# Performance work log

Measured on AMD Instinct MI355X. Metric: run time of the kernel, lower is better.

## Reference

```python
import jax, jax.numpy as jnp
import numpy as np

NEG_CAUSAL = -1e10  # matches torch buffer triu(ones*-1e10, diag=1)
NEG_PAD = -10000.0
NUM_HEADS = 16


def setup_inputs() -> dict:
    key = jax.random.key(0)
    ks = jax.random.split(key, 6)
    B, S, D = 2, 2048, 1024
    scale = 0.02
    return {
        "hidden_states": jax.random.normal(ks[0], (B, S, D), jnp.float32),
        "attention_mask": jnp.ones((B, S), jnp.float32),
        "Wq": jax.random.normal(ks[1], (D, D), jnp.float32) * scale,
        "bq": jnp.zeros((D,), jnp.float32),
        "Wk": jax.random.normal(ks[2], (D, D), jnp.float32) * scale,
        "bk": jnp.zeros((D,), jnp.float32),
        "Wv": jax.random.normal(ks[3], (D, D), jnp.float32) * scale,
        "bv": jnp.zeros((D,), jnp.float32),
        "Wo": jax.random.normal(ks[4], (D, D), jnp.float32) * scale,
        "bo": jnp.zeros((D,), jnp.float32),
    }


def reference(hidden_states, attention_mask, Wq, bq, Wk, bk, Wv, bv, Wo, bo):
    B, S, D = hidden_states.shape
    H = NUM_HEADS
    hd = D // H

    def heads(x):  # [B,S,D] -> [B,H,S,hd]
        return x.reshape(B, S, H, hd).transpose(0, 2, 1, 3)

    q = heads(hidden_states @ Wq + bq)
    k = heads(hidden_states @ Wk + bk)
    v = heads(hidden_states @ Wv + bv)

    scores = jnp.einsum("bhqd,bhkd->bhqk", q, k) / jnp.sqrt(jnp.float32(hd))
    causal = jnp.triu(jnp.full((S, S), NEG_CAUSAL, jnp.float32), k=1)
    scores = scores + causal
    # additive padding mask: (1 - m) * -10000, broadcast over heads and query pos
    scores = scores + (1.0 - attention_mask)[:, None, None, :] * NEG_PAD

    probs = jax.nn.softmax(scores, axis=-1)
    # dropout p=0.1 is inactive in eval mode (training=False)
    ctx = jnp.einsum("bhqk,bhkd->bhqd", probs, v)
    ctx = ctx.transpose(0, 2, 1, 3).reshape(B, S, D)
    return ctx @ Wo + bo
```

## Files before the change

### kernel.cpp

```cpp
#include <hip/hip_runtime.h>

typedef __attribute__((ext_vector_type(8))) short short8_t;
typedef __attribute__((ext_vector_type(4))) float float4_t;
typedef unsigned short u16;
typedef unsigned int u32;
typedef unsigned long long u64;

__device__ inline u16 f2bf(float x) {
  union { float f; u32 u; } v; v.f = x;
  u32 r = v.u + 0x7FFFu + ((v.u >> 16) & 1u);
  return (u16)(r >> 16);
}
#if __has_builtin(__builtin_amdgcn_cvt_pk_bf16_f32)
typedef __attribute__((ext_vector_type(2))) __bf16 bf162_t;
__device__ inline u32 pk2(float a, float b) {
  union { bf162_t v; u32 u; } cv;
  cv.v = __builtin_amdgcn_cvt_pk_bf16_f32(a, b);
  return cv.u;
}
#else
__device__ inline u32 pk2(float a, float b) {
  return (u32)f2bf(a) | ((u32)f2bf(b) << 16);
}
#endif

__global__ __launch_bounds__(256) void prologue(const float* __restrict__ X,
                                                const float* __restrict__ Wq, const float* __restrict__ Wk,
                                                const float* __restrict__ Wv, const float* __restrict__ Wo,
                                                u16* __restrict__ Xb, u16* __restrict__ WqkvT,
                                                u16* __restrict__ WoT, const float* __restrict__ maskp,
                                                u32* __restrict__ flags) {
  __shared__ float tls[32][33];
  int bid = blockIdx.x;
  if (bid < 4096) {
    int i = bid * 256 + threadIdx.x;
    float4_t x = ((const float4_t*)X)[i];
    union { u32 u[2]; u64 ll; } o;
    o.u[0] = pk2(x[0], x[1]);
    o.u[1] = pk2(x[2], x[3]);
    ((u64*)Xb)[i] = o.ll;
  } else if (bid < 8192) {
    int t = bid - 4096;
    int mat = t >> 10, tile = t & 1023;
    const float* W = (mat == 0) ? Wq : (mat == 1) ? Wk : (mat == 2) ? Wv : Wo;
    u16* WT = (mat < 3) ? WqkvT + ((size_t)mat << 20) : WoT;
    int tx = threadIdx.x & 31, ty = threadIdx.x >> 5;
    int c0 = (tile & 31) * 32, r0 = (tile >> 5) * 32;
    #pragma unroll
    for (int i = 0; i < 4; ++i)
      tls[ty + i * 8][tx] = W[(r0 + ty + i * 8) * 1024 + c0 + tx];
    __syncthreads();
    #pragma unroll
    for (int i = 0; i < 4; ++i)
      WT[(size_t)(c0 + ty + i * 8) * 1024 + r0 + tx] = f2bf(tls[tx][ty + i * 8]);
  } else {
    int b = bid - 8192;
    const float* mb = maskp + (b << 11) + threadIdx.x * 8;
    bool ok = true;
    #pragma unroll
    for (int i = 0; i < 8; ++i) ok &= (mb[i] == 1.0f);
    u64 bal = __ballot(ok);
    int w = threadIdx.x >> 6;
    if ((threadIdx.x & 63) == 0) tls[0][w] = (bal == ~0ull) ? 1.0f : 0.0f;
    __syncthreads();
    if (threadIdx.x == 0)
      flags[b] = (tls[0][0] != 0.0f && tls[0][1] != 0.0f &&
                  tls[0][2] != 0.0f && tls[0][3] != 0.0f) ? 1u : 0u;
  }
}

__global__ __launch_bounds__(256) void gemm128(const u16* __restrict__ A, const u16* __restrict__ BT,
                                               const float* __restrict__ bias0, const float* __restrict__ bias1,
                                               const float* __restrict__ bias2,
                                               void* __restrict__ o0, void* __restrict__ o1, void* __restrict__ o2,
                                               int mode) {
  __shared__ __align__(16) u16 Als[128 * 64];
  __shared__ __align__(16) u16 Bls[128 * 64];
  int g = blockIdx.x, m0t, n0t;
  if (mode == 4) {
    int mh = g / 384, r = g - mh * 384;
    n0t = r >> 4;
    m0t = mh * 16 + (r & 15);
  } else {
    m0t = g & 31;
    n0t = g >> 5;
  }
  const int m0 = m0t * 128, n0 = n0t * 128;
  const int lane = threadIdx.x & 63, wave = threadIdx.x >> 6;
  const int quad = lane >> 4, c = lane & 15;
  const int wm = wave >> 1, wn = wave & 1;

  const int srow = lane >> 3, schunk = lane & 7;
  int soff[4], dst[4];
  #pragma unroll
  for (int q = 0; q < 4; ++q) {
    int r = wave * 32 + q * 8 + srow;
    soff[q] = r * 1024 + (schunk << 3);
    dst[q]  = r * 64 + ((schunk ^ (r & 7)) << 3);
  }
  const u16* gA = A + (size_t)m0 * 1024;
  const u16* gB = BT + (size_t)n0 * 1024;

  int ar[2][4], br[2][4];
  #pragma unroll
  for (int ko = 0; ko < 2; ++ko) {
    #pragma unroll
    for (int i = 0; i < 4; ++i) {
      int rowa = wm * 64 + i * 16 + c;
      ar[ko][i] = rowa * 64 + (((ko * 4 + quad) ^ (rowa & 7)) << 3);
      int rowb = wn * 64 + i * 16 + c;
      br[ko][i] = rowb * 64 + (((ko * 4 + quad) ^ (rowb & 7)) << 3);
    }
  }

  short8_t ra[4], rb[4];
  #pragma unroll
  for (int q = 0; q < 4; ++q) ra[q] = *(const short8_t*)(gA + soff[q]);
  #pragma unroll
  for (int q = 0; q < 4; ++q) rb[q] = *(const short8_t*)(gB + soff[q]);

  float4_t acc[4][4] = {};
  for (int k0 = 0; k0 < 1024; k0 += 64) {
    #pragma unroll
    for (int q = 0; q < 4; ++q) *(short8_t*)&Als[dst[q]] = ra[q];
    #pragma unroll
    for (int q = 0; q < 4; ++q) *(short8_t*)&Bls[dst[q]] = rb[q];
    __syncthreads();
    if (k0 < 960) {
      #pragma unroll
      for (int q = 0; q < 4; ++q) ra[q] = *(const short8_t*)(gA + soff[q] + k0 + 64);
      #pragma unroll
      for (int q = 0; q < 4; ++q) rb[q] = *(const short8_t*)(gB + soff[q] + k0 + 64);
    }
    #pragma unroll
    for (int ko = 0; ko < 2; ++ko) {
      short8_t af[4], bfr[4];
      #pragma unroll
      for (int i = 0; i < 4; ++i) af[i] = *(const short8_t*)&Als[ar[ko][i]];
      #pragma unroll
      for (int j = 0; j < 4; ++j) bfr[j] = *(const short8_t*)&Bls[br[ko][j]];
      #pragma unroll
      for (int i = 0; i < 4; ++i)
        #pragma unroll
        for (int j = 0; j < 4; ++j)
          acc[i][j] = __builtin_amdgcn_mfma_f32_16x16x32_bf16(af[i], bfr[j], acc[i][j], 0, 0, 0);
    }
    __syncthreads();
  }

  const int mrow = m0 + wm * 64, ncol = n0 + wn * 64;
  if (mode == 3) {
    float* o = (float*)o0;
    #pragma unroll
    for (int i = 0; i < 4; ++i) {
      #pragma unroll
      for (int j = 0; j < 4; ++j) {
        int colb = ncol + j * 16 + c;
        float bv = bias0[colb];
        int rowb = mrow + i * 16 + quad * 4;
        #pragma unroll
        for (int r = 0; r < 4; ++r)
          o[(size_t)(rowb + r) * 1024 + colb] = acc[i][j][r] + bv;
      }
    }
  } else {
    #pragma unroll
    for (int j = 0; j < 4; ++j) {
      int colb = ncol + j * 16 + c;
      int which = colb >> 10;
      int n1 = colb & 1023, h = n1 >> 6, d = n1 & 63;
      const float* bp = (which == 0) ? bias0 : (which == 1 ? bias1 : bias2);
      float bv = bp[n1];
      #pragma unroll
      for (int i = 0; i < 4; ++i) {
        int rowb = mrow + i * 16 + quad * 4;
        int b = rowb >> 11, s = rowb & 2047;
        if (which == 2) {
          u16* o = (u16*)o2 + (((size_t)(b * 16 + h) * 64 + d) * 2048 + s);
          union { u32 u[2]; u64 ll; } ov;
          ov.u[0] = pk2(acc[i][j][0] + bv, acc[i][j][1] + bv);
          ov.u[1] = pk2(acc[i][j][2] + bv, acc[i][j][3] + bv);
          *(u64*)o = ov.ll;
        } else {
          float sc = (which == 0) ? 0.18033688011112042f : 1.0f;
          u16* o = (u16*)((which == 0) ? o0 : o1);
          #pragma unroll
          for (int r = 0; r < 4; ++r)
            o[(((size_t)(b * 16 + h) * 2048 + (s + r)) << 6) + d] = f2bf((acc[i][j][r] + bv) * sc);
        }
      }
    }
  }
}

__device__ inline short8_t p_to_b_swap(const float* p) {
  u32 a0 = pk2(p[0], p[1]), a1 = pk2(p[2], p[3]);
  u32 b0 = pk2(p[4], p[5]), b1 = pk2(p[6], p[7]);
  asm("v_permlane32_swap_b32 %0, %1" : "+v"(a0), "+v"(b0));
  asm("v_permlane32_swap_b32 %0, %1" : "+v"(a1), "+v"(b1));
  asm("v_permlane16_swap_b32 %0, %1" : "+v"(a0), "+v"(b0));
  asm("v_permlane16_swap_b32 %0, %1" : "+v"(a1), "+v"(b1));
  union { u32 u[4]; short8_t v; } pf;
  pf.u[0] = a0; pf.u[1] = a1; pf.u[2] = b0; pf.u[3] = b1;
  return pf.v;
}

__global__ __launch_bounds__(256, 4) void attn_kernel(const u16* __restrict__ Q, const u16* __restrict__ K,
                                                      const u16* __restrict__ VT, const float* __restrict__ mask,
                                                      const u32* __restrict__ flags, u16* __restrict__ ctx) {
  __shared__ __align__(16) u16 Kls[2 * 64 * 64];
  __shared__ __align__(16) u16 Vls[2 * 64 * 64];
  const float C1 = 10000.0f * 1.4426950408889634f;
  int w = threadIdx.x >> 6, lane = threadIdx.x & 63;
  int quad = lane >> 4, c = lane & 15;
  int g = blockIdx.x;
  int bh = (g & 7) * 4 + ((g >> 3) & 3);
  int u = g >> 5;
  int qt = (u < 16) ? (31 - u) : (u - 16);
  int b = bh >> 4, h = bh & 15;
  bool ones = flags && (flags[b] != 0);
  const u16* Kp = K + ((size_t)bh << 17);
  const u16* Vp = VT + ((size_t)bh << 17);
  const float* mp = mask + (b << 11);
  int q0 = qt * 64 + w * 16;

  const u16* Qp = Q + (((size_t)bh * 2048 + q0 + c) << 6) + quad * 8;
  short8_t qf0 = *(const short8_t*)(Qp);
  short8_t qf1 = *(const short8_t*)(Qp + 32);

  const int srow = lane >> 3, schunk = lane & 7;
  const u16* gK[2]; const u16* gV[2]; int dK[2], dV[2];
  #pragma unroll
  for (int i = 0; i < 2; ++i) {
    int R = w * 16 + i * 8 + srow;
    gK[i] = Kp + R * 64 + (schunk << 3);
    dK[i] = R * 64 + ((schunk ^ (R & 7)) << 3);
    gV[i] = Vp + (size_t)R * 2048 + (schunk << 3);
    dV[i] = R * 64 + ((schunk ^ (R & 7)) << 3);
  }

  int koff[4][2];
  #pragma unroll
  for (int kg = 0; kg < 4; ++kg) {
    int r = kg * 16 + c;
    #pragma unroll
    for (int ko = 0; ko < 2; ++ko)
      koff[kg][ko] = r * 64 + (((ko * 4 + quad) ^ (r & 7)) << 3);
  }
  int voff[4][2];
  #pragma unroll
  for (int dblk = 0; dblk < 4; ++dblk) {
    int d = dblk * 16 + c;
    #pragma unroll
    for (int kc = 0; kc < 2; ++kc)
      voff[dblk][kc] = d * 64 + (((kc * 4 + quad) ^ (d & 7)) << 3);
  }

  int ke[8];
  #pragma unroll
  for (int e = 0; e < 8; ++e) ke[e] = ((e >> 2) << 4) + quad * 4 + (e & 3);
  int thr = w * 16 + c;

  float4_t O[4] = {};
  float l = 0.0f;

  short8_t kreg[2], vreg[2];
  #pragma unroll
  for (int i = 0; i < 2; ++i) { kreg[i] = *(const short8_t*)(gK[i]); vreg[i] = *(const short8_t*)(gV[i]); }

  for (int t = 0; t <= qt; ++t) {
    int kb = t << 6;
    int bufo = (t & 1) << 12;
    #pragma unroll
    for (int i = 0; i < 2; ++i) *(short8_t*)&Kls[bufo + dK[i]] = kreg[i];
    #pragma unroll
    for (int i = 0; i < 2; ++i) *(short8_t*)&Vls[bufo + dV[i]] = vreg[i];
    __syncthreads();
    if (t < qt) {
      int kb2 = (t + 1) << 6;
      #pragma unroll
      for (int i = 0; i < 2; ++i) {
        kreg[i] = *(const short8_t*)(gK[i] + (size_t)kb2 * 64);
        vreg[i] = *(const short8_t*)(gV[i] + kb2);
      }
    }
    float4_t s[4];
    #pragma unroll
    for (int kg = 0; kg < 4; ++kg) {
      short8_t k0 = *(const short8_t*)&Kls[bufo + koff[kg][0]];
      short8_t k1 = *(const short8_t*)&Kls[bufo + koff[kg][1]];
      float4_t a = {};
      a = __builtin_amdgcn_mfma_f32_16x16x32_bf16(k0, qf0, a, 0, 0, 0);
      a = __builtin_amdgcn_mfma_f32_16x16x32_bf16(k1, qf1, a, 0, 0, 0);
      s[kg] = a;
    }
    float4_t mpl[4];
    if (!ones) {
      #pragma unroll
      for (int kg = 0; kg < 4; ++kg)
        mpl[kg] = (*(const float4_t*)(mp + kb + kg * 16 + quad * 4) - 1.0f) * C1;
    }
    bool diag = (t == qt);
    short8_t pf[2];
    #pragma unroll
    for (int kc = 0; kc < 2; ++kc) {
      float p[8];
      #pragma unroll
      for (int e = 0; e < 8; ++e) {
        int kg = kc * 2 + (e >> 2);
        p[e] = s[kg][e & 3];
        if (!ones) p[e] += mpl[kg][e & 3];
      }
      if (diag) {
        #pragma unroll
        for (int e = 0; e < 8; ++e) {
          int ko2 = kc * 32 + ke[e];
          p[e] = (ko2 > thr) ? -50.0f : p[e];
        }
      }
      #pragma unroll
      for (int e = 0; e < 8; ++e) {
        float pe = exp2f(p[e]);
        p[e] = pe;
        l += pe;
      }
      pf[kc] = p_to_b_swap(p);
    }
    #pragma unroll
    for (int dblk = 0; dblk < 4; ++dblk) {
      #pragma unroll
      for (int kc = 0; kc < 2; ++kc) {
        short8_t vf = *(const short8_t*)&Vls[bufo + voff[dblk][kc]];
        O[dblk] = __builtin_amdgcn_mfma_f32_16x16x32_bf16(vf, pf[kc], O[dblk], 0, 0, 0);
      }
    }
  }
  l += __shfl_xor(l, 16);
  l += __shfl_xor(l, 32);
  float rl = 1.0f / l;
  u16* op = ctx + ((size_t)(b * 2048 + q0 + c) * 1024 + h * 64 + quad * 4);
  #pragma unroll
  for (int dblk = 0; dblk < 4; ++dblk) {
    union { u32 uu[2]; u64 ll; } ov;
    ov.uu[0] = pk2(O[dblk][0] * rl, O[dblk][1] * rl);
    ov.uu[1] = pk2(O[dblk][2] * rl, O[dblk][3] * rl);
    *(u64*)(op + dblk * 16) = ov.ll;
  }
}

extern "C" void kernel_launch(void* const* d_in, const int* in_sizes, int n_in,
                              void* d_out, int out_size, void* d_ws, size_t ws_size,
                              hipStream_t stream) {
  const float* X    = (const float*)d_in[0];
  const float* mask = (const float*)d_in[1];
  const float* Wq   = (const float*)d_in[2];
  const float* bq   = (const float*)d_in[3];
  const float* Wk   = (const float*)d_in[4];
  const float* bk   = (const float*)d_in[5];
  const float* Wv   = (const float*)d_in[6];
  const float* bv   = (const float*)d_in[7];
  const float* Wo   = (const float*)d_in[8];
  const float* bo   = (const float*)d_in[9];

  char* w = (char*)d_ws;
  u16* Xb     = (u16*)(w);
  u16* WqkvT  = (u16*)(w + (8ull  << 20));
  u16* WoT    = (u16*)(w + (14ull << 20));
  u16* Qb     = (u16*)(w + (16ull << 20));
  u16* Kb     = (u16*)(w + (24ull << 20));
  u16* VTb    = (u16*)(w + (32ull << 20));
  u16* Ctx    = (u16*)(w + (40ull << 20));
  u32* flags  = (ws_size >= (48ull << 20) + 8) ? (u32*)(w + (48ull << 20)) : nullptr;

  prologue<<<flags ? 8194 : 8192, 256, 0, stream>>>(X, Wq, Wk, Wv, Wo, Xb, WqkvT, WoT, mask, flags);
  gemm128<<<768, 256, 0, stream>>>(Xb, WqkvT, bq, bk, bv, Qb, Kb, VTb, 4);
  attn_kernel<<<1024, 256, 0, stream>>>(Qb, Kb, VTb, mask, flags, Ctx);
  gemm128<<<256, 256, 0, stream>>>(Ctx, WoT, bo, bo, bo, d_out, d_out, d_out, 3);
}
```

Baseline: 185.7 us.

## Load V fragments directly from global memory and add MFMA priority hints

```diff
diff --git a/kernel.cpp b/kernel.cpp
--- a/kernel.cpp
+++ b/kernel.cpp
@@ -209,7 +209,6 @@
                                                       const u16* __restrict__ VT, const float* __restrict__ mask,
                                                       const u32* __restrict__ flags, u16* __restrict__ ctx) {
   __shared__ __align__(16) u16 Kls[2 * 64 * 64];
-  __shared__ __align__(16) u16 Vls[2 * 64 * 64];
   const float C1 = 10000.0f * 1.4426950408889634f;
   int w = threadIdx.x >> 6, lane = threadIdx.x & 63;
   int quad = lane >> 4, c = lane & 15;
@@ -229,14 +228,12 @@
   short8_t qf1 = *(const short8_t*)(Qp + 32);
 
   const int srow = lane >> 3, schunk = lane & 7;
-  const u16* gK[2]; const u16* gV[2]; int dK[2], dV[2];
+  const u16* gK[2]; int dK[2];
   #pragma unroll
   for (int i = 0; i < 2; ++i) {
     int R = w * 16 + i * 8 + srow;
     gK[i] = Kp + R * 64 + (schunk << 3);
     dK[i] = R * 64 + ((schunk ^ (R & 7)) << 3);
-    gV[i] = Vp + (size_t)R * 2048 + (schunk << 3);
-    dV[i] = R * 64 + ((schunk ^ (R & 7)) << 3);
   }
 
   int koff[4][2];
@@ -247,14 +244,8 @@
     for (int ko = 0; ko < 2; ++ko)
       koff[kg][ko] = r * 64 + (((ko * 4 + quad) ^ (r & 7)) << 3);
   }
-  int voff[4][2];
-  #pragma unroll
-  for (int dblk = 0; dblk < 4; ++dblk) {
-    int d = dblk * 16 + c;
-    #pragma unroll
-    for (int kc = 0; kc < 2; ++kc)
-      voff[dblk][kc] = d * 64 + (((kc * 4 + quad) ^ (d & 7)) << 3);
-  }
+
+  const u16* vb0 = Vp + c * 2048 + quad * 8;
 
   int ke[8];
   #pragma unroll
@@ -264,27 +255,30 @@
   float4_t O[4] = {};
   float l = 0.0f;
 
-  short8_t kreg[2], vreg[2];
-  #pragma unroll
-  for (int i = 0; i < 2; ++i) { kreg[i] = *(const short8_t*)(gK[i]); vreg[i] = *(const short8_t*)(gV[i]); }
+  short8_t kreg[2];
+  #pragma unroll
+  for (int i = 0; i < 2; ++i) kreg[i] = *(const short8_t*)(gK[i]);
 
   for (int t = 0; t <= qt; ++t) {
     int kb = t << 6;
     int bufo = (t & 1) << 12;
     #pragma unroll
     for (int i = 0; i < 2; ++i) *(short8_t*)&Kls[bufo + dK[i]] = kreg[i];
-    #pragma unroll
-    for (int i = 0; i < 2; ++i) *(short8_t*)&Vls[bufo + dV[i]] = vreg[i];
-    __syncthreads();
+    __syncthreads();
+    short8_t vf[4][2];
+    #pragma unroll
+    for (int dblk = 0; dblk < 4; ++dblk)
+      #pragma unroll
+      for (int kc = 0; kc < 2; ++kc)
+        vf[dblk][kc] = *(const short8_t*)(vb0 + (size_t)dblk * 16 * 2048 + kb + kc * 32);
     if (t < qt) {
       int kb2 = (t + 1) << 6;
       #pragma unroll
-      for (int i = 0; i < 2; ++i) {
+      for (int i = 0; i < 2; ++i)
         kreg[i] = *(const short8_t*)(gK[i] + (size_t)kb2 * 64);
-        vreg[i] = *(const short8_t*)(gV[i] + kb2);
-      }
     }
     float4_t s[4];
+    __builtin_amdgcn_s_setprio(1);
     #pragma unroll
     for (int kg = 0; kg < 4; ++kg) {
       short8_t k0 = *(const short8_t*)&Kls[bufo + koff[kg][0]];
@@ -294,6 +288,7 @@
       a = __builtin_amdgcn_mfma_f32_16x16x32_bf16(k1, qf1, a, 0, 0, 0);
       s[kg] = a;
     }
+    __builtin_amdgcn_s_setprio(0);
     float4_t mpl[4];
     if (!ones) {
       #pragma unroll
@@ -326,14 +321,13 @@
       }
       pf[kc] = p_to_b_swap(p);
     }
+    __builtin_amdgcn_s_setprio(1);
     #pragma unroll
     for (int dblk = 0; dblk < 4; ++dblk) {
-      #pragma unroll
-      for (int kc = 0; kc < 2; ++kc) {
-        short8_t vf = *(const short8_t*)&Vls[bufo + voff[dblk][kc]];
-        O[dblk] = __builtin_amdgcn_mfma_f32_16x16x32_bf16(vf, pf[kc], O[dblk], 0, 0, 0);
-      }
-    }
+      O[dblk] = __builtin_amdgcn_mfma_f32_16x16x32_bf16(vf[dblk][0], pf[0], O[dblk], 0, 0, 0);
+      O[dblk] = __builtin_amdgcn_mfma_f32_16x16x32_bf16(vf[dblk][1], pf[1], O[dblk], 0, 0, 0);
+    }
+    __builtin_amdgcn_s_setprio(0);
   }
   l += __shfl_xor(l, 16);
   l += __shfl_xor(l, 32);
```

Measured after the change: 215.5 us. +16.0%, slower.

## Use 128-query attention tiles with 8 waves and MFMA row-sum

Applied to the files above, without the earlier changes.

```diff
diff --git a/kernel.cpp b/kernel.cpp
--- a/kernel.cpp
+++ b/kernel.cpp
@@ -205,7 +205,7 @@
   return pf.v;
 }
 
-__global__ __launch_bounds__(256, 4) void attn_kernel(const u16* __restrict__ Q, const u16* __restrict__ K,
+__global__ __launch_bounds__(512, 4) void attn_kernel(const u16* __restrict__ Q, const u16* __restrict__ K,
                                                       const u16* __restrict__ VT, const float* __restrict__ mask,
                                                       const u32* __restrict__ flags, u16* __restrict__ ctx) {
   __shared__ __align__(16) u16 Kls[2 * 64 * 64];
@@ -216,28 +216,23 @@
   int g = blockIdx.x;
   int bh = (g & 7) * 4 + ((g >> 3) & 3);
   int u = g >> 5;
-  int qt = (u < 16) ? (31 - u) : (u - 16);
+  int qt16 = (u < 8) ? (15 - u) : (u - 8);
   int b = bh >> 4, h = bh & 15;
   bool ones = flags && (flags[b] != 0);
   const u16* Kp = K + ((size_t)bh << 17);
   const u16* Vp = VT + ((size_t)bh << 17);
   const float* mp = mask + (b << 11);
-  int q0 = qt * 64 + w * 16;
+  int q0 = qt16 * 128 + w * 16;
+  int nt = 2 * qt16 + 2;
 
   const u16* Qp = Q + (((size_t)bh * 2048 + q0 + c) << 6) + quad * 8;
   short8_t qf0 = *(const short8_t*)(Qp);
   short8_t qf1 = *(const short8_t*)(Qp + 32);
 
-  const int srow = lane >> 3, schunk = lane & 7;
-  const u16* gK[2]; const u16* gV[2]; int dK[2], dV[2];
-  #pragma unroll
-  for (int i = 0; i < 2; ++i) {
-    int R = w * 16 + i * 8 + srow;
-    gK[i] = Kp + R * 64 + (schunk << 3);
-    dK[i] = R * 64 + ((schunk ^ (R & 7)) << 3);
-    gV[i] = Vp + (size_t)R * 2048 + (schunk << 3);
-    dV[i] = R * 64 + ((schunk ^ (R & 7)) << 3);
-  }
+  const int srow = threadIdx.x >> 3, schunk = threadIdx.x & 7;
+  const u16* gK = Kp + srow * 64 + (schunk << 3);
+  const u16* gV = Vp + (size_t)srow * 2048 + (schunk << 3);
+  const int dst = srow * 64 + ((schunk ^ (srow & 7)) << 3);
 
   int koff[4][2];
   #pragma unroll
@@ -259,32 +254,29 @@
   int ke[8];
   #pragma unroll
   for (int e = 0; e < 8; ++e) ke[e] = ((e >> 2) << 4) + quad * 4 + (e & 3);
-  int thr = w * 16 + c;
+  int thr = q0 + c;
 
   float4_t O[4] = {};
-  float l = 0.0f;
-
-  short8_t kreg[2], vreg[2];
-  #pragma unroll
-  for (int i = 0; i < 2; ++i) { kreg[i] = *(const short8_t*)(gK[i]); vreg[i] = *(const short8_t*)(gV[i]); }
-
-  for (int t = 0; t <= qt; ++t) {
+  float4_t l4 = {};
+  union { u32 uu[4]; short8_t v; } onesf;
+  onesf.uu[0] = onesf.uu[1] = onesf.uu[2] = onesf.uu[3] = 0x3F803F80u;
+
+  short8_t kreg = *(const short8_t*)(gK);
+  short8_t vreg = *(const short8_t*)(gV);
+
+  for (int t = 0; t < nt; ++t) {
     int kb = t << 6;
     int bufo = (t & 1) << 12;
-    #pragma unroll
-    for (int i = 0; i < 2; ++i) *(short8_t*)&Kls[bufo + dK[i]] = kreg[i];
-    #pragma unroll
-    for (int i = 0; i < 2; ++i) *(short8_t*)&Vls[bufo + dV[i]] = vreg[i];
-    __syncthreads();
-    if (t < qt) {
+    *(short8_t*)&Kls[bufo + dst] = kreg;
+    *(short8_t*)&Vls[bufo + dst] = vreg;
+    __syncthreads();
+    if (t < nt - 1) {
       int kb2 = (t + 1) << 6;
-      #pragma unroll
-      for (int i = 0; i < 2; ++i) {
-        kreg[i] = *(const short8_t*)(gK[i] + (size_t)kb2 * 64);
-        vreg[i] = *(const short8_t*)(gV[i] + kb2);
-      }
+      kreg = *(const short8_t*)(gK + (size_t)kb2 * 64);
+      vreg = *(const short8_t*)(gV + kb2);
     }
     float4_t s[4];
+    __builtin_amdgcn_s_setprio(1);
     #pragma unroll
     for (int kg = 0; kg < 4; ++kg) {
       short8_t k0 = *(const short8_t*)&Kls[bufo + koff[kg][0]];
@@ -294,13 +286,14 @@
       a = __builtin_amdgcn_mfma_f32_16x16x32_bf16(k1, qf1, a, 0, 0, 0);
       s[kg] = a;
     }
+    __builtin_amdgcn_s_setprio(0);
     float4_t mpl[4];
     if (!ones) {
       #pragma unroll
       for (int kg = 0; kg < 4; ++kg)
         mpl[kg] = (*(const float4_t*)(mp + kb + kg * 16 + quad * 4) - 1.0f) * C1;
     }
-    bool diag = (t == qt);
+    bool diag = (kb + 63 > q0);
     short8_t pf[2];
     #pragma unroll
     for (int kc = 0; kc < 2; ++kc) {
@@ -314,18 +307,15 @@
       if (diag) {
         #pragma unroll
         for (int e = 0; e < 8; ++e) {
-          int ko2 = kc * 32 + ke[e];
-          p[e] = (ko2 > thr) ? -50.0f : p[e];
+          int keyg = kb + kc * 32 + ke[e];
+          p[e] = (keyg > thr) ? -50.0f : p[e];
         }
       }
       #pragma unroll
-      for (int e = 0; e < 8; ++e) {
-        float pe = exp2f(p[e]);
-        p[e] = pe;
-        l += pe;
-      }
+      for (int e = 0; e < 8; ++e) p[e] = exp2f(p[e]);
       pf[kc] = p_to_b_swap(p);
     }
+    __builtin_amdgcn_s_setprio(1);
     #pragma unroll
     for (int dblk = 0; dblk < 4; ++dblk) {
       #pragma unroll
@@ -334,10 +324,11 @@
         O[dblk] = __builtin_amdgcn_mfma_f32_16x16x32_bf16(vf, pf[kc], O[dblk], 0, 0, 0);
       }
     }
-  }
-  l += __shfl_xor(l, 16);
-  l += __shfl_xor(l, 32);
-  float rl = 1.0f / l;
+    l4 = __builtin_amdgcn_mfma_f32_16x16x32_bf16(onesf.v, pf[0], l4, 0, 0, 0);
+    l4 = __builtin_amdgcn_mfma_f32_16x16x32_bf16(onesf.v, pf[1], l4, 0, 0, 0);
+    __builtin_amdgcn_s_setprio(0);
+  }
+  float rl = 1.0f / l4[0];
   u16* op = ctx + ((size_t)(b * 2048 + q0 + c) * 1024 + h * 64 + quad * 4);
   #pragma unroll
   for (int dblk = 0; dblk < 4; ++dblk) {
@@ -374,6 +365,6 @@
 
   prologue<<<flags ? 8194 : 8192, 256, 0, stream>>>(X, Wq, Wk, Wv, Wo, Xb, WqkvT, WoT, mask, flags);
   gemm128<<<768, 256, 0, stream>>>(Xb, WqkvT, bq, bk, bv, Qb, Kb, VTb, 4);
-  attn_kernel<<<1024, 256, 0, stream>>>(Qb, Kb, VTb, mask, flags, Ctx);
+  attn_kernel<<<512, 512, 0, stream>>>(Qb, Kb, VTb, mask, flags, Ctx);
   gemm128<<<256, 256, 0, stream>>>(Ctx, WoT, bo, bo, bo, d_out, d_out, d_out, 3);
 }
```

After: 190.7 us. 2.7% more time.

## Split long causal query tiles across blocks and merge partials in output GEMM

Applied to the files above, without the earlier changes.

```diff
diff --git a/kernel.cpp b/kernel.cpp
--- a/kernel.cpp
+++ b/kernel.cpp
@@ -2,6 +2,7 @@
 
 typedef __attribute__((ext_vector_type(8))) short short8_t;
 typedef __attribute__((ext_vector_type(4))) float float4_t;
+typedef __attribute__((ext_vector_type(8))) _Float16 half8_t;
 typedef unsigned short u16;
 typedef unsigned int u32;
 typedef unsigned long long u64;
@@ -69,11 +70,34 @@
   }
 }
 
+__device__ inline short8_t load_ctx_row(const u16* __restrict__ A, int r, int col0,
+                                        const u16* __restrict__ Op1h, const u16* __restrict__ Op2h,
+                                        const float* __restrict__ lp1, const float* __restrict__ lp2) {
+  if (!(r & 1024))
+    return *(const short8_t*)(A + (size_t)r * 1024 + col0);
+  int b = r >> 11, s = r & 2047;
+  int hh = col0 >> 6, d0 = col0 & 63;
+  int qt = s >> 6, jj = 31 - qt, q = s & 63;
+  int slot = (((b << 4) + hh) << 4) + jj;
+  size_t off = ((size_t)slot * 64 + q) * 64 + d0;
+  half8_t o1 = *(const half8_t*)(Op1h + off);
+  half8_t o2 = *(const half8_t*)(Op2h + off);
+  float rl = 1.0f / (lp1[slot * 64 + q] + lp2[slot * 64 + q]);
+  union { u32 u[4]; short8_t v; } ov;
+  #pragma unroll
+  for (int e = 0; e < 4; ++e)
+    ov.u[e] = pk2(((float)o1[2 * e] + (float)o2[2 * e]) * rl,
+                  ((float)o1[2 * e + 1] + (float)o2[2 * e + 1]) * rl);
+  return ov.v;
+}
+
 __global__ __launch_bounds__(256) void gemm128(const u16* __restrict__ A, const u16* __restrict__ BT,
                                                const float* __restrict__ bias0, const float* __restrict__ bias1,
                                                const float* __restrict__ bias2,
                                                void* __restrict__ o0, void* __restrict__ o1, void* __restrict__ o2,
-                                               int mode) {
+                                               int mode,
+                                               const u16* __restrict__ Op1h, const u16* __restrict__ Op2h,
+                                               const float* __restrict__ lp1, const float* __restrict__ lp2) {
   __shared__ __align__(16) u16 Als[128 * 64];
   __shared__ __align__(16) u16 Bls[128 * 64];
   int g = blockIdx.x, m0t, n0t;
@@ -91,12 +115,13 @@
   const int wm = wave >> 1, wn = wave & 1;
 
   const int srow = lane >> 3, schunk = lane & 7;
-  int soff[4], dst[4];
+  int soff[4], dst[4], rrow[4];
   #pragma unroll
   for (int q = 0; q < 4; ++q) {
     int r = wave * 32 + q * 8 + srow;
     soff[q] = r * 1024 + (schunk << 3);
     dst[q]  = r * 64 + ((schunk ^ (r & 7)) << 3);
+    rrow[q] = m0 + r;
   }
   const u16* gA = A + (size_t)m0 * 1024;
   const u16* gB = BT + (size_t)n0 * 1024;
@@ -114,8 +139,13 @@
   }
 
   short8_t ra[4], rb[4];
-  #pragma unroll
-  for (int q = 0; q < 4; ++q) ra[q] = *(const short8_t*)(gA + soff[q]);
+  if (mode == 3) {
+    #pragma unroll
+    for (int q = 0; q < 4; ++q) ra[q] = load_ctx_row(A, rrow[q], schunk << 3, Op1h, Op2h, lp1, lp2);
+  } else {
+    #pragma unroll
+    for (int q = 0; q < 4; ++q) ra[q] = *(const short8_t*)(gA + soff[q]);
+  }
   #pragma unroll
   for (int q = 0; q < 4; ++q) rb[q] = *(const short8_t*)(gB + soff[q]);
 
@@ -127,8 +157,14 @@
     for (int q = 0; q < 4; ++q) *(short8_t*)&Bls[dst[q]] = rb[q];
     __syncthreads();
     if (k0 < 960) {
-      #pragma unroll
-      for (int q = 0; q < 4; ++q) ra[q] = *(const short8_t*)(gA + soff[q] + k0 + 64);
+      if (mode == 3) {
+        #pragma unroll
+        for (int q = 0; q < 4; ++q)
+          ra[q] = load_ctx_row(A, rrow[q], k0 + 64 + (schunk << 3), Op1h, Op2h, lp1, lp2);
+      } else {
+        #pragma unroll
+        for (int q = 0; q < 4; ++q) ra[q] = *(const short8_t*)(gA + soff[q] + k0 + 64);
+      }
       #pragma unroll
       for (int q = 0; q < 4; ++q) rb[q] = *(const short8_t*)(gB + soff[q] + k0 + 64);
     }
@@ -207,7 +243,9 @@
 
 __global__ __launch_bounds__(256, 4) void attn_kernel(const u16* __restrict__ Q, const u16* __restrict__ K,
                                                       const u16* __restrict__ VT, const float* __restrict__ mask,
-                                                      const u32* __restrict__ flags, u16* __restrict__ ctx) {
+                                                      const u32* __restrict__ flags, u16* __restrict__ ctx,
+                                                      u16* __restrict__ Op1h, u16* __restrict__ Op2h,
+                                                      float* __restrict__ lp1, float* __restrict__ lp2) {
   __shared__ __align__(16) u16 Kls[2 * 64 * 64];
   __shared__ __align__(16) u16 Vls[2 * 64 * 64];
   const float C1 = 10000.0f * 1.4426950408889634f;
@@ -215,18 +253,22 @@
   int quad = lane >> 4, c = lane & 15;
   int g = blockIdx.x;
   int bh = (g & 7) * 4 + ((g >> 3) & 3);
-  int u = g >> 5;
-  int qt = (u < 16) ? (31 - u) : (u - 16);
+  int wid = g >> 5;
+  int j = wid & 15;
+  bool isB = (wid < 16);
+  int qa = 31 - j;
   int b = bh >> 4, h = bh & 15;
   bool ones = flags && (flags[b] != 0);
   const u16* Kp = K + ((size_t)bh << 17);
   const u16* Vp = VT + ((size_t)bh << 17);
   const float* mp = mask + (b << 11);
-  int q0 = qt * 64 + w * 16;
-
-  const u16* Qp = Q + (((size_t)bh * 2048 + q0 + c) << 6) + quad * 8;
-  short8_t qf0 = *(const short8_t*)(Qp);
-  short8_t qf1 = *(const short8_t*)(Qp + 32);
+
+  int nseg = isB ? 2 : 1;
+  int sq[2], slo[2], shi[2], spr[2];
+  if (isB) { sq[0] = qa; slo[0] = 16; shi[0] = 32 - j; spr[0] = 2;
+             sq[1] = j;  slo[1] = 0;  shi[1] = j + 1;  spr[1] = 0; }
+  else     { sq[0] = qa; slo[0] = 0;  shi[0] = 16;     spr[0] = 1;
+             sq[1] = 0;  slo[1] = 0;  shi[1] = 0;      spr[1] = 0; }
 
   const int srow = lane >> 3, schunk = lane & 7;
   const u16* gK[2]; const u16* gV[2]; int dK[2], dV[2];
@@ -260,91 +302,124 @@
   #pragma unroll
   for (int e = 0; e < 8; ++e) ke[e] = ((e >> 2) << 4) + quad * 4 + (e & 3);
   int thr = w * 16 + c;
-
-  float4_t O[4] = {};
-  float l = 0.0f;
+  union { u32 uu[4]; short8_t v; } onesf;
+  onesf.uu[0] = onesf.uu[1] = onesf.uu[2] = onesf.uu[3] = 0x3F803F80u;
 
   short8_t kreg[2], vreg[2];
-  #pragma unroll
-  for (int i = 0; i < 2; ++i) { kreg[i] = *(const short8_t*)(gK[i]); vreg[i] = *(const short8_t*)(gV[i]); }
-
-  for (int t = 0; t <= qt; ++t) {
-    int kb = t << 6;
-    int bufo = (t & 1) << 12;
-    #pragma unroll
-    for (int i = 0; i < 2; ++i) *(short8_t*)&Kls[bufo + dK[i]] = kreg[i];
-    #pragma unroll
-    for (int i = 0; i < 2; ++i) *(short8_t*)&Vls[bufo + dV[i]] = vreg[i];
-    __syncthreads();
-    if (t < qt) {
-      int kb2 = (t + 1) << 6;
-      #pragma unroll
-      for (int i = 0; i < 2; ++i) {
-        kreg[i] = *(const short8_t*)(gK[i] + (size_t)kb2 * 64);
-        vreg[i] = *(const short8_t*)(gV[i] + kb2);
-      }
-    }
-    float4_t s[4];
-    #pragma unroll
-    for (int kg = 0; kg < 4; ++kg) {
-      short8_t k0 = *(const short8_t*)&Kls[bufo + koff[kg][0]];
-      short8_t k1 = *(const short8_t*)&Kls[bufo + koff[kg][1]];
-      float4_t a = {};
-      a = __builtin_amdgcn_mfma_f32_16x16x32_bf16(k0, qf0, a, 0, 0, 0);
-      a = __builtin_amdgcn_mfma_f32_16x16x32_bf16(k1, qf1, a, 0, 0, 0);
-      s[kg] = a;
-    }
-    float4_t mpl[4];
-    if (!ones) {
-      #pragma unroll
-      for (int kg = 0; kg < 4; ++kg)
-        mpl[kg] = (*(const float4_t*)(mp + kb + kg * 16 + quad * 4) - 1.0f) * C1;
-    }
-    bool diag = (t == qt);
-    short8_t pf[2];
-    #pragma unroll
-    for (int kc = 0; kc < 2; ++kc) {
-      float p[8];
-      #pragma unroll
-      for (int e = 0; e < 8; ++e) {
-        int kg = kc * 2 + (e >> 2);
-        p[e] = s[kg][e & 3];
-        if (!ones) p[e] += mpl[kg][e & 3];
-      }
-      if (diag) {
+  {
+    int kb0 = slo[0] << 6;
+    #pragma unroll
+    for (int i = 0; i < 2; ++i) {
+      kreg[i] = *(const short8_t*)(gK[i] + (size_t)kb0 * 64);
+      vreg[i] = *(const short8_t*)(gV[i] + kb0);
+    }
+  }
+
+  int tt = 0;
+  for (int seg = 0; seg < nseg; ++seg) {
+    const int qt = sq[seg], klo = slo[seg], khi = shi[seg], par = spr[seg];
+    const int q0 = qt * 64 + w * 16;
+    const u16* Qp = Q + (((size_t)bh * 2048 + q0 + c) << 6) + quad * 8;
+    short8_t qf0 = *(const short8_t*)(Qp);
+    short8_t qf1 = *(const short8_t*)(Qp + 32);
+    float4_t O[4] = {};
+    float4_t l4 = {};
+
+    for (int t = klo; t < khi; ++t, ++tt) {
+      int kb = t << 6;
+      int bufo = (tt & 1) << 12;
+      #pragma unroll
+      for (int i = 0; i < 2; ++i) *(short8_t*)&Kls[bufo + dK[i]] = kreg[i];
+      #pragma unroll
+      for (int i = 0; i < 2; ++i) *(short8_t*)&Vls[bufo + dV[i]] = vreg[i];
+      __syncthreads();
+      int nk = (t + 1 < khi) ? ((t + 1) << 6) : ((seg + 1 < nseg) ? (slo[seg + 1] << 6) : -1);
+      if (nk >= 0) {
+        #pragma unroll
+        for (int i = 0; i < 2; ++i) {
+          kreg[i] = *(const short8_t*)(gK[i] + (size_t)nk * 64);
+          vreg[i] = *(const short8_t*)(gV[i] + nk);
+        }
+      }
+      float4_t s[4];
+      __builtin_amdgcn_s_setprio(1);
+      #pragma unroll
+      for (int kg = 0; kg < 4; ++kg) {
+        short8_t k0 = *(const short8_t*)&Kls[bufo + koff[kg][0]];
+        short8_t k1 = *(const short8_t*)&Kls[bufo + koff[kg][1]];
+        float4_t a = {};
+        a = __builtin_amdgcn_mfma_f32_16x16x32_bf16(k0, qf0, a, 0, 0, 0);
+        a = __builtin_amdgcn_mfma_f32_16x16x32_bf16(k1, qf1, a, 0, 0, 0);
+        s[kg] = a;
+      }
+      __builtin_amdgcn_s_setprio(0);
+      float4_t mpl[4];
+      if (!ones) {
+        #pragma unroll
+        for (int kg = 0; kg < 4; ++kg)
+          mpl[kg] = (*(const float4_t*)(mp + kb + kg * 16 + quad * 4) - 1.0f) * C1;
+      }
+      bool diag = (t == qt);
+      short8_t pf[2];
+      #pragma unroll
+      for (int kc = 0; kc < 2; ++kc) {
+        float p[8];
         #pragma unroll
         for (int e = 0; e < 8; ++e) {
-          int ko2 = kc * 32 + ke[e];
-          p[e] = (ko2 > thr) ? -50.0f : p[e];
+          int kg = kc * 2 + (e >> 2);
+          p[e] = s[kg][e & 3];
+          if (!ones) p[e] += mpl[kg][e & 3];
         }
-      }
-      #pragma unroll
-      for (int e = 0; e < 8; ++e) {
-        float pe = exp2f(p[e]);
-        p[e] = pe;
-        l += pe;
-      }
-      pf[kc] = p_to_b_swap(p);
-    }
-    #pragma unroll
-    for (int dblk = 0; dblk < 4; ++dblk) {
-      #pragma unroll
-      for (int kc = 0; kc < 2; ++kc) {
-        short8_t vf = *(const short8_t*)&Vls[bufo + voff[dblk][kc]];
-        O[dblk] = __builtin_amdgcn_mfma_f32_16x16x32_bf16(vf, pf[kc], O[dblk], 0, 0, 0);
-      }
-    }
-  }
-  l += __shfl_xor(l, 16);
-  l += __shfl_xor(l, 32);
-  float rl = 1.0f / l;
-  u16* op = ctx + ((size_t)(b * 2048 + q0 + c) * 1024 + h * 64 + quad * 4);
-  #pragma unroll
-  for (int dblk = 0; dblk < 4; ++dblk) {
-    union { u32 uu[2]; u64 ll; } ov;
-    ov.uu[0] = pk2(O[dblk][0] * rl, O[dblk][1] * rl);
-    ov.uu[1] = pk2(O[dblk][2] * rl, O[dblk][3] * rl);
-    *(u64*)(op + dblk * 16) = ov.ll;
+        if (diag) {
+          #pragma unroll
+          for (int e = 0; e < 8; ++e) {
+            int ko2 = kc * 32 + ke[e];
+            p[e] = (ko2 > thr) ? -50.0f : p[e];
+          }
+        }
+        #pragma unroll
+        for (int e = 0; e < 8; ++e) p[e] = exp2f(p[e]);
+        pf[kc] = p_to_b_swap(p);
+      }
+      __builtin_amdgcn_s_setprio(1);
+      #pragma unroll
+      for (int dblk = 0; dblk < 4; ++dblk) {
+        #pragma unroll
+        for (int kc = 0; kc < 2; ++kc) {
+          short8_t vf = *(const short8_t*)&Vls[bufo + voff[dblk][kc]];
+          O[dblk] = __builtin_amdgcn_mfma_f32_16x16x32_bf16(vf, pf[kc], O[dblk], 0, 0, 0);
+        }
+      }
+      l4 = __builtin_amdgcn_mfma_f32_16x16x32_bf16(onesf.v, pf[0], l4, 0, 0, 0);
+      l4 = __builtin_amdgcn_mfma_f32_16x16x32_bf16(onesf.v, pf[1], l4, 0, 0, 0);
+      __builtin_amdgcn_s_setprio(0);
+    }
+
+    if (par == 0) {
+      float rl = 1.0f / l4[0];
+      u16* op = ctx + ((size_t)(b * 2048 + q0 + c) * 1024 + h * 64 + quad * 4);
+      #pragma unroll
+      for (int dblk = 0; dblk < 4; ++dblk) {
+        union { u32 uu[2]; u64 ll; } ov;
+        ov.uu[0] = pk2(O[dblk][0] * rl, O[dblk][1] * rl);
+        ov.uu[1] = pk2(O[dblk][2] * rl, O[dblk][3] * rl);
+        *(u64*)(op + dblk * 16) = ov.ll;
+      }
+    } else {
+      u16* Op = (par == 1) ? Op1h : Op2h;
+      float* lp = (par == 1) ? lp1 : lp2;
+      int slot = (bh << 4) + j;
+      int ql = w * 16 + c;
+      size_t base = ((size_t)slot * 64 + ql) * 64 + quad * 4;
+      #pragma unroll
+      for (int dblk = 0; dblk < 4; ++dblk) {
+        union { _Float16 hv[4]; u64 ll; } pv;
+        #pragma unroll
+        for (int r = 0; r < 4; ++r) pv.hv[r] = (_Float16)O[dblk][r];
+        *(u64*)(Op + base + dblk * 16) = pv.ll;
+      }
+      if (quad == 0) lp[slot * 64 + ql] = l4[0];
+    }
   }
 }
 
@@ -371,9 +446,15 @@
   u16* VTb    = (u16*)(w + (32ull << 20));
   u16* Ctx    = (u16*)(w + (40ull << 20));
   u32* flags  = (ws_size >= (48ull << 20) + 8) ? (u32*)(w + (48ull << 20)) : nullptr;
+  u16*   Op1h = (u16*)(w);
+  u16*   Op2h = (u16*)(w + (4ull << 20));
+  float* lp1  = (float*)(w + (8ull << 20));
+  float* lp2  = (float*)(w + (8ull << 20) + (256ull << 10));
 
   prologue<<<flags ? 8194 : 8192, 256, 0, stream>>>(X, Wq, Wk, Wv, Wo, Xb, WqkvT, WoT, mask, flags);
-  gemm128<<<768, 256, 0, stream>>>(Xb, WqkvT, bq, bk, bv, Qb, Kb, VTb, 4);
-  attn_kernel<<<1024, 256, 0, stream>>>(Qb, Kb, VTb, mask, flags, Ctx);
-  gemm128<<<256, 256, 0, stream>>>(Ctx, WoT, bo, bo, bo, d_out, d_out, d_out, 3);
-}
+  gemm128<<<768, 256, 0, stream>>>(Xb, WqkvT, bq, bk, bv, Qb, Kb, VTb, 4,
+                                   nullptr, nullptr, nullptr, nullptr);
+  attn_kernel<<<1024, 256, 0, stream>>>(Qb, Kb, VTb, mask, flags, Ctx, Op1h, Op2h, lp1, lp2);
+  gemm128<<<256, 256, 0, stream>>>(Ctx, WoT, bo, bo, bo, d_out, d_out, d_out, 3,
+                                   Op1h, Op2h, lp1, lp2);
+}
```

Result: slower. 212.0 us (+14.2%).
